# Kernel optimization log

Hardware: AMD Instinct MI355X
Metric: run time of the kernel (lower is better)

## Reference

```python
import jax, jax.numpy as jnp
import numpy as np

N_USERS = 100000
N_ITEMS = 50000
EMB = 64
E_U = 1600000
E_I = 800000
EPS = 1e-12
NEG_SLOPE = 0.01  # torch F.leaky_relu default


def _spmm(rows, cols, vals, x, n):
    # sparse.mm(adj, x): out[r] += vals[e] * x[cols[e]] for each edge e with rows[e]==r
    return jax.ops.segment_sum(vals[:, None] * x[cols], rows, num_segments=n)


def _l2norm(x):
    # F.normalize(x, p=2, dim=1)
    n = jnp.sqrt(jnp.sum(x * x, axis=1, keepdims=True))
    return x / jnp.maximum(n, EPS)


def setup_inputs() -> dict:
    key = jax.random.key(0)
    ks = jax.random.split(key, 16)
    inp = {
        'user_emb': 0.01 * jax.random.normal(ks[0], (N_USERS, EMB), jnp.float32),
        'item_emb': 0.01 * jax.random.normal(ks[1], (N_ITEMS, EMB), jnp.float32),
        'Wu0': jax.random.normal(ks[2], (EMB, EMB), jnp.float32) / np.sqrt(EMB),
        'bu0': jnp.zeros((EMB,), jnp.float32),
        'Wu1': jax.random.normal(ks[3], (EMB, EMB), jnp.float32) / np.sqrt(EMB),
        'bu1': jnp.zeros((EMB,), jnp.float32),
        'Wi0': jax.random.normal(ks[4], (EMB, EMB), jnp.float32) / np.sqrt(EMB),
        'bi0': jnp.zeros((EMB,), jnp.float32),
        'Wi1': jax.random.normal(ks[5], (EMB, EMB), jnp.float32) / np.sqrt(EMB),
        'bi1': jnp.zeros((EMB,), jnp.float32),
        'u_rows': jax.random.randint(ks[6], (E_U,), 0, N_USERS, jnp.int32),
        'u_cols': jax.random.randint(ks[7], (E_U,), 0, N_USERS, jnp.int32),
        'u_vals': jax.random.uniform(ks[8], (E_U,), jnp.float32) / 16.0,
        'i_rows': jax.random.randint(ks[9], (E_I,), 0, N_ITEMS, jnp.int32),
        'i_cols': jax.random.randint(ks[10], (E_I,), 0, N_ITEMS, jnp.int32),
        'i_vals': jax.random.uniform(ks[11], (E_I,), jnp.float32) / 16.0,
    }
    return inp


def reference(user_emb, item_emb, Wu0, bu0, Wu1, bu1, Wi0, bi0, Wi1, bi1,
              u_rows, u_cols, u_vals, i_rows, i_cols, i_vals):
    u = user_emb
    i = item_emb
    u_w = [(Wu0, bu0), (Wu1, bu1)]
    i_w = [(Wi0, bi0), (Wi1, bi1)]
    for l in range(2):
        Wu, bu = u_w[l]
        Wi, bi = i_w[l]
        u = _spmm(u_rows, u_cols, u_vals, u, N_USERS)
        u = jax.nn.leaky_relu(u @ Wu.T + bu, NEG_SLOPE)
        u = _l2norm(u)  # dropout p=0 -> identity
        i = _spmm(i_rows, i_cols, i_vals, i, N_ITEMS)
        i = jax.nn.leaky_relu(i @ Wi.T + bi, NEG_SLOPE)
        i = _l2norm(i)
    return (u, i)
```

## Files before the change

### kernel.cpp

```cpp
#include <hip/hip_runtime.h>
#include <hip/hip_bf16.h>
#include <math.h>

#define EMB 64
#define CAPB 3584
#define CHUNK 4096

typedef __attribute__((ext_vector_type(8))) short bf16x8;
typedef __attribute__((ext_vector_type(4))) float f32x4;

__device__ __forceinline__ ushort bf16_rne(float f) {
    uint u = __float_as_uint(f);
    return (ushort)((u + 0x7fffu + ((u >> 16) & 1u)) >> 16);
}


__device__ __forceinline__ void bin_body(
    const int* __restrict__ rows, const int* __restrict__ cols,
    const float* __restrict__ vals, int nE, int B, int RPB,
    int* gcur, int2* __restrict__ binned, int blk,
    int* cnt, int* sstart, int* lbase, int2* rec, ushort* bkt) {
    int t = threadIdx.x;
    for (int i = t; i < B; i += 256) cnt[i] = 0;
    __syncthreads();
    int c0 = blk * CHUNK;
    int ntot = nE - c0; if (ntot > CHUNK) ntot = CHUNK;
    int bs[16];
#pragma unroll
    for (int j = 0; j < 16; ++j) {
        int idx = c0 + t + j * 256;
        int bsv = -1;
        if (idx < nE) {
            int row = rows[idx];
            int b = row / RPB;
            int inrow = row - b * RPB;
            int slot = atomicAdd(&cnt[b], 1);
            bsv = (b << 21) | (inrow << 13) | slot;
        }
        bs[j] = bsv;
    }
    __syncthreads();
    for (int i = t; i < B; i += 256) {
        int c = cnt[i];
        lbase[i] = c ? atomicAdd(&gcur[i * 16], c) : 0;
    }
    if (t < 64) {
        int carry = 0;
        int nseg = B >> 6;
        for (int seg = 0; seg < nseg; ++seg) {
            int i = seg * 64 + t;
            int v = cnt[i];
            int s = v;
#pragma unroll
            for (int d = 1; d < 64; d <<= 1) {
                int u2 = __shfl_up(s, d);
                if (t >= d) s += u2;
            }
            sstart[i] = carry + s - v;
            carry += __shfl(s, 63);
        }
    }
    __syncthreads();
#pragma unroll
    for (int j = 0; j < 16; ++j) {
        int idx = c0 + t + j * 256;
        if (idx >= nE) continue;
        int bsv = bs[j];
        int b = bsv >> 21, inrow = (bsv >> 13) & 0xFF, slot = bsv & 0x1FFF;
        int col = cols[idx];
        float v = vals[idx];
        int li = sstart[b] + slot;
        rec[li] = make_int2(col | (inrow << 17), __float_as_int(v));
        bkt[li] = (ushort)b;
    }
    __syncthreads();
    for (int i = t; i < ntot; i += 256) {
        int b = bkt[i];
        int pos = lbase[b] + (i - sstart[b]);
        if (pos < CAPB)
            binned[(size_t)b * CAPB + pos] = rec[i];
    }
}

__global__ __launch_bounds__(256) void prep(
    const int* __restrict__ u_rows, const int* __restrict__ u_cols,
    const float* __restrict__ u_vals, int eu, int BU, int RPBU,
    int* gcurU, int2* __restrict__ binnedU, int nbU,
    const int* __restrict__ i_rows, const int* __restrict__ i_cols,
    const float* __restrict__ i_vals, int ei, int BI, int RPBI,
    int* gcurI, int2* __restrict__ binnedI, int nbI,
    const float4* __restrict__ embU, ushort* __restrict__ xbU, long n4u,
    const float4* __restrict__ embI, ushort* __restrict__ xbI, long n4i,
    int nbCast) {
    __shared__ int2 rec[CHUNK];
    __shared__ ushort bkt[CHUNK];
    __shared__ int cnt[512];
    __shared__ int sstart[512];
    __shared__ int lbase[512];
    int b = blockIdx.x;
    if (b < nbU) {
        bin_body(u_rows, u_cols, u_vals, eu, BU, RPBU, gcurU, binnedU, b,
                 cnt, sstart, lbase, rec, bkt);
        return;
    }
    b -= nbU;
    if (b < nbI) {
        bin_body(i_rows, i_cols, i_vals, ei, BI, RPBI, gcurI, binnedI, b,
                 cnt, sstart, lbase, rec, bkt);
        return;
    }
    b -= nbI;
    long tot = n4u + n4i;
    long base = (long)b * 1024 + threadIdx.x;
#pragma unroll
    for (int k = 0; k < 4; ++k) {
        long i = base + k * 256;
        if (i >= tot) return;
        const float4* a; ushort* o; long j;
        if (i < n4u) { a = embU; o = xbU; j = i; }
        else { a = embI; o = xbI; j = i - n4u; }
        float4 v = a[j];
        ushort4 r;
        r.x = bf16_rne(v.x); r.y = bf16_rne(v.y); r.z = bf16_rne(v.z); r.w = bf16_rne(v.w);
        *(ushort4*)(o + j * 4) = r;
    }
}

__device__ __forceinline__ int block_scan_1024(int v, int* wsum) {
    int tid = threadIdx.x, lane = tid & 63, wid = tid >> 6;
    int s = v;
#pragma unroll
    for (int d = 1; d < 64; d <<= 1) {
        int t = __shfl_up(s, d);
        if (lane >= d) s += t;
    }
    if (lane == 63) wsum[wid] = s;
    __syncthreads();
    if (tid < 16) {
        int ws = wsum[tid];
#pragma unroll
        for (int d = 1; d < 16; d <<= 1) {
            int t = __shfl_up(ws, d);
            if (tid >= d) ws += t;
        }
        wsum[tid] = ws;
    }
    __syncthreads();
    int wpref = (wid > 0) ? wsum[wid - 1] : 0;
    return wpref + s;
}

__global__ void scan_buckets(const int* __restrict__ gcurU, int BU, int* cntbU, int* ebaseU,
                             const int* __restrict__ gcurI, int BI, int* cntbI, int* ebaseI) {
    __shared__ int wsum[16];
    const int* gcur; int B; int* cntb; int* ebase;
    if (blockIdx.x == 0) { gcur = gcurU; B = BU; cntb = cntbU; ebase = ebaseU; }
    else { gcur = gcurI; B = BI; cntb = cntbI; ebase = ebaseI; }
    int t = threadIdx.x;
    int v = 0;
    if (t < B) {
        v = gcur[t * 16];
        if (v < 0) v = 0;
        if (v > CAPB) v = CAPB;
    }
    int incl = block_scan_1024(v, wsum);
    if (t < B) { cntb[t] = v; ebase[t] = incl - v; }
}

__global__ __launch_bounds__(256) void finalize_csr(
    const int2* __restrict__ binnedU, const int* __restrict__ cntbU,
    const int* __restrict__ ebaseU, int RPBU, int nu,
    int2* __restrict__ ccvU, int* __restrict__ uoff, int BU,
    const int2* __restrict__ binnedI, const int* __restrict__ cntbI,
    const int* __restrict__ ebaseI, int RPBI, int ni,
    int2* __restrict__ ccvI, int* __restrict__ ioff) {
    __shared__ int2 rec[CAPB];
    __shared__ int cnt_r[256];
    __shared__ int excl[257];
    __shared__ int curs[256];
    int b = blockIdx.x;
    const int2* binned; const int* cntb; const int* ebase; int RPB; int n;
    int2* ccv; int* off;
    if (b < BU) {
        binned = binnedU; cntb = cntbU; ebase = ebaseU; RPB = RPBU; n = nu;
        ccv = ccvU; off = uoff;
    } else {
        b -= BU;
        binned = binnedI; cntb = cntbI; ebase = ebaseI; RPB = RPBI; n = ni;
        ccv = ccvI; off = ioff;
    }
    int t = threadIdx.x;
    int r0 = b * RPB;
    int nrows = n - r0; if (nrows > RPB) nrows = RPB;
    if (nrows <= 0) return;
    int cnt = cntb[b];
    int eb  = ebase[b];
    const int2* src = binned + (size_t)b * CAPB;
    cnt_r[t] = 0;
    __syncthreads();
    for (int p = t; p < cnt; p += 256) {
        int2 r = src[p];
        rec[p] = r;
        atomicAdd(&cnt_r[(r.x >> 17) & 0xFF], 1);
    }
    __syncthreads();
    if (t < 64) {
        int carry = 0;
#pragma unroll
        for (int seg = 0; seg < 4; ++seg) {
            int i = seg * 64 + t;
            int v = cnt_r[i];
            int s = v;
#pragma unroll
            for (int d = 1; d < 64; d <<= 1) {
                int u2 = __shfl_up(s, d);
                if (t >= d) s += u2;
            }
            excl[i] = carry + s - v;
            carry += __shfl(s, 63);
        }
        if (t == 0) excl[256] = carry;
    }
    __syncthreads();
    curs[t] = excl[t];
    if (t < nrows) off[r0 + t] = eb + excl[t];
    if (t == 0 && r0 + nrows == n) off[n] = eb + cnt;
    __syncthreads();
    for (int p = t; p < cnt; p += 256) {
        int2 r = rec[p];
        int inrow = (r.x >> 17) & 0xFF;
        int slot = atomicAdd(&curs[inrow], 1);
        ccv[eb + slot] = make_int2(r.x & 0x1FFFF, r.y);
    }
}


__global__ __launch_bounds__(256, 4) void spmm_mfma(
    const int* __restrict__ uoff, const int2* __restrict__ ccvU,
    const ushort* __restrict__ xu, const float* __restrict__ Wu, const float* __restrict__ bu,
    float* __restrict__ yfu, ushort* __restrict__ ybu, int nu, int ntU,
    const int* __restrict__ ioff, const int2* __restrict__ ccvI,
    const ushort* __restrict__ xi, const float* __restrict__ Wi, const float* __restrict__ bi,
    float* __restrict__ yfi, ushort* __restrict__ ybi, int ni) {
    __shared__ ushort wt[64 * 72];
    __shared__ ushort xt[4 * 16 * 72];
    int tid = threadIdx.x;
    int lane = tid & 63, wid = tid >> 6;
    int q = lane & 15, g = lane >> 4;
    int tile = blockIdx.x;
    const int* off; const int2* ccv; const ushort* x; const float* W; const float* bv;
    float* yf; ushort* yb; int n;
    if (tile < ntU) {
        off = uoff; ccv = ccvU; x = xu; W = Wu; bv = bu; yf = yfu; yb = ybu; n = nu;
    } else {
        tile -= ntU;
        off = ioff; ccv = ccvI; x = xi; W = Wi; bv = bi; yf = yfi; yb = ybi; n = ni;
    }
    for (int idx = tid; idx < EMB * EMB; idx += 256) {
        int r = idx >> 6, c = idx & 63;
        wt[r * 72 + c] = bf16_rne(W[idx]);
    }
    float bias[4];
#pragma unroll
    for (int t = 0; t < 4; ++t) bias[t] = bv[16 * t + q];
    __syncthreads();

    const uint2* xv2 = (const uint2*)x;
    ushort* xw = xt + wid * (16 * 72);
    int rowW = (tile << 6) + wid * 16;

#pragma unroll
    for (int j = 0; j < 4; ++j) {
        int rr = j * 4 + g;
        int row = rowW + rr;
        float av[4] = {0.f, 0.f, 0.f, 0.f};
        if (row < n) {
            int s = off[row], e = off[row + 1];
            for (int p = s; p < e; p += 8) {
                int2 ed[8];
                uint2 gx[8];
#pragma unroll
                for (int k = 0; k < 8; ++k) {
                    int idx = p + k;
                    idx = (idx < e) ? idx : (e - 1);
                    ed[k] = ccv[idx];
                }
#pragma unroll
                for (int k = 0; k < 8; ++k)
                    gx[k] = xv2[(size_t)(uint)ed[k].x * 16 + q];
#pragma unroll
                for (int k = 0; k < 8; ++k) {
                    float v = (p + k < e) ? __int_as_float(ed[k].y) : 0.f;
                    av[0] = fmaf(v, __uint_as_float(gx[k].x << 16), av[0]);
                    av[1] = fmaf(v, __uint_as_float(gx[k].x & 0xffff0000u), av[1]);
                    av[2] = fmaf(v, __uint_as_float(gx[k].y << 16), av[2]);
                    av[3] = fmaf(v, __uint_as_float(gx[k].y & 0xffff0000u), av[3]);
                }
            }
        }
        uint p0 = (uint)bf16_rne(av[0]) | ((uint)bf16_rne(av[1]) << 16);
        uint p1 = (uint)bf16_rne(av[2]) | ((uint)bf16_rne(av[3]) << 16);
        *(uint2*)(xw + rr * 72 + q * 4) = make_uint2(p0, p1);
    }
    __syncthreads();

    f32x4 ac0 = {0.f, 0.f, 0.f, 0.f}, ac1 = ac0, ac2 = ac0, ac3 = ac0;
#pragma unroll
    for (int ks = 0; ks < 2; ++ks) {
        bf16x8 af = *(const bf16x8*)(xw + q * 72 + g * 8 + ks * 32);
        bf16x8 b0 = *(const bf16x8*)(wt + (q +  0) * 72 + g * 8 + ks * 32);
        bf16x8 b1 = *(const bf16x8*)(wt + (q + 16) * 72 + g * 8 + ks * 32);
        bf16x8 b2 = *(const bf16x8*)(wt + (q + 32) * 72 + g * 8 + ks * 32);
        bf16x8 b3 = *(const bf16x8*)(wt + (q + 48) * 72 + g * 8 + ks * 32);
        ac0 = __builtin_amdgcn_mfma_f32_16x16x32_bf16(af, b0, ac0, 0, 0, 0);
        ac1 = __builtin_amdgcn_mfma_f32_16x16x32_bf16(af, b1, ac1, 0, 0, 0);
        ac2 = __builtin_amdgcn_mfma_f32_16x16x32_bf16(af, b2, ac2, 0, 0, 0);
        ac3 = __builtin_amdgcn_mfma_f32_16x16x32_bf16(af, b3, ac3, 0, 0, 0);
    }

    float dv[4][4];
    float ss[4] = {0.f, 0.f, 0.f, 0.f};
#pragma unroll
    for (int t = 0; t < 4; ++t) {
        f32x4 a = (t == 0) ? ac0 : (t == 1) ? ac1 : (t == 2) ? ac2 : ac3;
#pragma unroll
        for (int r = 0; r < 4; ++r) {
            float d = a[r] + bias[t];
            d = (d > 0.f) ? d : 0.01f * d;
            dv[t][r] = d;
            ss[r] = fmaf(d, d, ss[r]);
        }
    }
#pragma unroll
    for (int r = 0; r < 4; ++r) {
        float s2 = ss[r];
        s2 += __shfl_xor(s2, 1);
        s2 += __shfl_xor(s2, 2);
        s2 += __shfl_xor(s2, 4);
        s2 += __shfl_xor(s2, 8);
        float scl = 1.0f / fmaxf(sqrtf(s2), 1e-12f);
        int orow = rowW + g * 4 + r;
        if (orow < n) {
#pragma unroll
            for (int t = 0; t < 4; ++t) {
                float outv = dv[t][r] * scl;
                size_t cidx = (size_t)orow * EMB + 16 * t + q;
                if (yb) yb[cidx] = bf16_rne(outv);
                else    yf[cidx] = outv;
            }
        }
    }
}


extern "C" void kernel_launch(void* const* d_in, const int* in_sizes, int n_in,
                              void* d_out, int out_size, void* d_ws, size_t ws_size,
                              hipStream_t stream) {
    const float* user_emb = (const float*)d_in[0];
    const float* item_emb = (const float*)d_in[1];
    const float* Wu0 = (const float*)d_in[2];
    const float* bu0 = (const float*)d_in[3];
    const float* Wu1 = (const float*)d_in[4];
    const float* bu1 = (const float*)d_in[5];
    const float* Wi0 = (const float*)d_in[6];
    const float* bi0 = (const float*)d_in[7];
    const float* Wi1 = (const float*)d_in[8];
    const float* bi1 = (const float*)d_in[9];
    const int*   u_rows = (const int*)d_in[10];
    const int*   u_cols = (const int*)d_in[11];
    const float* u_vals = (const float*)d_in[12];
    const int*   i_rows = (const int*)d_in[13];
    const int*   i_cols = (const int*)d_in[14];
    const float* i_vals = (const float*)d_in[15];

    const int nu = in_sizes[0] / EMB;
    const int ni = in_sizes[1] / EMB;
    const int eu = in_sizes[10];
    const int ei = in_sizes[13];

    const int BU = 512, BI = 256;
    const int RPBU = (nu + BU - 1) / BU;
    const int RPBI = (ni + BI - 1) / BI;

    float* out_u = (float*)d_out;
    float* out_i = out_u + (size_t)nu * EMB;

    size_t o = 0;
    char* wsb = (char*)d_ws;
    auto carve = [&](size_t bytes) -> void* {
        void* p = wsb + o;
        o += (bytes + 255) & ~(size_t)255;
        return p;
    };
    ushort* xbu0 = (ushort*)carve((size_t)nu * EMB * 2);
    ushort* xbi0 = (ushort*)carve((size_t)ni * EMB * 2);
    size_t binnedU_bytes = (size_t)BU * CAPB * 8;
    size_t binnedI_bytes = (size_t)BI * CAPB * 8;
    size_t xb1_bytes = ((size_t)nu + ni) * EMB * 2;
    size_t shared_bytes = binnedU_bytes + binnedI_bytes;
    if (xb1_bytes > shared_bytes) shared_bytes = xb1_bytes;
    char* regionA = (char*)carve(shared_bytes);
    int2* binnedU = (int2*)regionA;
    int2* binnedI = (int2*)(regionA + binnedU_bytes);
    ushort* xbu1 = (ushort*)regionA;
    ushort* xbi1 = (ushort*)(regionA + (size_t)nu * EMB * 2);
    int2* ccvU  = (int2*)carve((size_t)eu * 8);
    int2* ccvI  = (int2*)carve((size_t)ei * 8);
    int*  uoff  = (int*)carve((size_t)(nu + 1) * 4);
    int*  ioff  = (int*)carve((size_t)(ni + 1) * 4);
    int*  gcur  = (int*)carve((size_t)(BU + BI) * 16 * 4);
    int*  gcurU = gcur;
    int*  gcurI = gcur + (size_t)BU * 16;
    int*  cntbU = (int*)carve((size_t)BU * 4);
    int*  ebaseU= (int*)carve((size_t)BU * 4);
    int*  cntbI = (int*)carve((size_t)BI * 4);
    int*  ebaseI= (int*)carve((size_t)BI * 4);
    (void)ws_size;

    hipMemsetAsync(gcur, 0, (size_t)(BU + BI) * 16 * 4, stream);
    {
        int nbU = (eu + CHUNK - 1) / CHUNK;
        int nbI = (ei + CHUNK - 1) / CHUNK;
        long n4u = (long)nu * EMB / 4, n4i = (long)ni * EMB / 4;
        int nbCast = (int)((n4u + n4i + 1023) / 1024);
        prep<<<nbU + nbI + nbCast, 256, 0, stream>>>(
            u_rows, u_cols, u_vals, eu, BU, RPBU, gcurU, binnedU, nbU,
            i_rows, i_cols, i_vals, ei, BI, RPBI, gcurI, binnedI, nbI,
            (const float4*)user_emb, xbu0, n4u,
            (const float4*)item_emb, xbi0, n4i, nbCast);
    }
    scan_buckets<<<2, 1024, 0, stream>>>(gcurU, BU, cntbU, ebaseU,
                                         gcurI, BI, cntbI, ebaseI);
    finalize_csr<<<BU + BI, 256, 0, stream>>>(
        binnedU, cntbU, ebaseU, RPBU, nu, ccvU, uoff, BU,
        binnedI, cntbI, ebaseI, RPBI, ni, ccvI, ioff);

    int ntU = (nu + 63) >> 6, ntI = (ni + 63) >> 6;
    spmm_mfma<<<ntU + ntI, 256, 0, stream>>>(
        uoff, ccvU, xbu0, Wu0, bu0, nullptr, xbu1, nu, ntU,
        ioff, ccvI, xbi0, Wi0, bi0, nullptr, xbi1, ni);
    spmm_mfma<<<ntU + ntI, 256, 0, stream>>>(
        uoff, ccvU, xbu1, Wu1, bu1, out_u, nullptr, nu, ntU,
        ioff, ccvI, xbi1, Wi1, bi1, out_i, nullptr, ni);
}
```

Baseline: 195.2 us.

## Drop bucket scan kernel and sort CSR in place within padded bins

Removes the scan_buckets launch and the compacted CCV arrays: finalize_csr now reads each bucket's count straight from gcur, sorts edges in place inside the padded binned buffer, and writes per-row (start,end) int2 pairs instead of a global offset array. The SpMM kernels read edges directly from the padded bins using these pairs. This drops one kernel launch and one serialized dependency. The xb1 buffers no longer alias the binned region, which raises workspace use. spmm launch bounds are also raised from 4 to 6 blocks per SM, which may limit registers.

```diff
diff --git a/kernel.cpp b/kernel.cpp
--- a/kernel.cpp
+++ b/kernel.cpp
@@ -126,76 +126,32 @@
     }
 }
 
-__device__ __forceinline__ int block_scan_1024(int v, int* wsum) {
-    int tid = threadIdx.x, lane = tid & 63, wid = tid >> 6;
-    int s = v;
-#pragma unroll
-    for (int d = 1; d < 64; d <<= 1) {
-        int t = __shfl_up(s, d);
-        if (lane >= d) s += t;
-    }
-    if (lane == 63) wsum[wid] = s;
-    __syncthreads();
-    if (tid < 16) {
-        int ws = wsum[tid];
-#pragma unroll
-        for (int d = 1; d < 16; d <<= 1) {
-            int t = __shfl_up(ws, d);
-            if (tid >= d) ws += t;
-        }
-        wsum[tid] = ws;
-    }
-    __syncthreads();
-    int wpref = (wid > 0) ? wsum[wid - 1] : 0;
-    return wpref + s;
-}
-
-__global__ void scan_buckets(const int* __restrict__ gcurU, int BU, int* cntbU, int* ebaseU,
-                             const int* __restrict__ gcurI, int BI, int* cntbI, int* ebaseI) {
-    __shared__ int wsum[16];
-    const int* gcur; int B; int* cntb; int* ebase;
-    if (blockIdx.x == 0) { gcur = gcurU; B = BU; cntb = cntbU; ebase = ebaseU; }
-    else { gcur = gcurI; B = BI; cntb = cntbI; ebase = ebaseI; }
-    int t = threadIdx.x;
-    int v = 0;
-    if (t < B) {
-        v = gcur[t * 16];
-        if (v < 0) v = 0;
-        if (v > CAPB) v = CAPB;
-    }
-    int incl = block_scan_1024(v, wsum);
-    if (t < B) { cntb[t] = v; ebase[t] = incl - v; }
-}
 
 __global__ __launch_bounds__(256) void finalize_csr(
-    const int2* __restrict__ binnedU, const int* __restrict__ cntbU,
-    const int* __restrict__ ebaseU, int RPBU, int nu,
-    int2* __restrict__ ccvU, int* __restrict__ uoff, int BU,
-    const int2* __restrict__ binnedI, const int* __restrict__ cntbI,
-    const int* __restrict__ ebaseI, int RPBI, int ni,
-    int2* __restrict__ ccvI, int* __restrict__ ioff) {
+    int2* __restrict__ binnedU, const int* __restrict__ gcurU, int RPBU, int nu,
+    int2* __restrict__ offseU, int BU,
+    int2* __restrict__ binnedI, const int* __restrict__ gcurI, int RPBI, int ni,
+    int2* __restrict__ offseI) {
     __shared__ int2 rec[CAPB];
     __shared__ int cnt_r[256];
     __shared__ int excl[257];
     __shared__ int curs[256];
     int b = blockIdx.x;
-    const int2* binned; const int* cntb; const int* ebase; int RPB; int n;
-    int2* ccv; int* off;
+    int2* binned; const int* gcur; int RPB; int n; int2* offse;
     if (b < BU) {
-        binned = binnedU; cntb = cntbU; ebase = ebaseU; RPB = RPBU; n = nu;
-        ccv = ccvU; off = uoff;
+        binned = binnedU; gcur = gcurU; RPB = RPBU; n = nu; offse = offseU;
     } else {
         b -= BU;
-        binned = binnedI; cntb = cntbI; ebase = ebaseI; RPB = RPBI; n = ni;
-        ccv = ccvI; off = ioff;
+        binned = binnedI; gcur = gcurI; RPB = RPBI; n = ni; offse = offseI;
     }
     int t = threadIdx.x;
     int r0 = b * RPB;
     int nrows = n - r0; if (nrows > RPB) nrows = RPB;
     if (nrows <= 0) return;
-    int cnt = cntb[b];
-    int eb  = ebase[b];
-    const int2* src = binned + (size_t)b * CAPB;
+    int cnt = gcur[b * 16];
+    if (cnt > CAPB) cnt = CAPB;
+    int2* src = binned + (size_t)b * CAPB;
+    int B0 = b * CAPB;
     cnt_r[t] = 0;
     __syncthreads();
     for (int p = t; p < cnt; p += 256) {
@@ -223,23 +179,22 @@
     }
     __syncthreads();
     curs[t] = excl[t];
-    if (t < nrows) off[r0 + t] = eb + excl[t];
-    if (t == 0 && r0 + nrows == n) off[n] = eb + cnt;
+    if (t < nrows) offse[r0 + t] = make_int2(B0 + excl[t], B0 + excl[t + 1]);
     __syncthreads();
     for (int p = t; p < cnt; p += 256) {
         int2 r = rec[p];
         int inrow = (r.x >> 17) & 0xFF;
         int slot = atomicAdd(&curs[inrow], 1);
-        ccv[eb + slot] = make_int2(r.x & 0x1FFFF, r.y);
-    }
-}
-
-
-__global__ __launch_bounds__(256, 4) void spmm_mfma(
-    const int* __restrict__ uoff, const int2* __restrict__ ccvU,
+        src[slot] = make_int2(r.x & 0x1FFFF, r.y);
+    }
+}
+
+
+__global__ __launch_bounds__(256, 6) void spmm_mfma(
+    const int2* __restrict__ offseU, const int2* __restrict__ ccvU,
     const ushort* __restrict__ xu, const float* __restrict__ Wu, const float* __restrict__ bu,
     float* __restrict__ yfu, ushort* __restrict__ ybu, int nu, int ntU,
-    const int* __restrict__ ioff, const int2* __restrict__ ccvI,
+    const int2* __restrict__ offseI, const int2* __restrict__ ccvI,
     const ushort* __restrict__ xi, const float* __restrict__ Wi, const float* __restrict__ bi,
     float* __restrict__ yfi, ushort* __restrict__ ybi, int ni) {
     __shared__ ushort wt[64 * 72];
@@ -248,13 +203,13 @@
     int lane = tid & 63, wid = tid >> 6;
     int q = lane & 15, g = lane >> 4;
     int tile = blockIdx.x;
-    const int* off; const int2* ccv; const ushort* x; const float* W; const float* bv;
+    const int2* offse; const int2* ccv; const ushort* x; const float* W; const float* bv;
     float* yf; ushort* yb; int n;
     if (tile < ntU) {
-        off = uoff; ccv = ccvU; x = xu; W = Wu; bv = bu; yf = yfu; yb = ybu; n = nu;
+        offse = offseU; ccv = ccvU; x = xu; W = Wu; bv = bu; yf = yfu; yb = ybu; n = nu;
     } else {
         tile -= ntU;
-        off = ioff; ccv = ccvI; x = xi; W = Wi; bv = bi; yf = yfi; yb = ybi; n = ni;
+        offse = offseI; ccv = ccvI; x = xi; W = Wi; bv = bi; yf = yfi; yb = ybi; n = ni;
     }
     for (int idx = tid; idx < EMB * EMB; idx += 256) {
         int r = idx >> 6, c = idx & 63;
@@ -275,7 +230,8 @@
         int row = rowW + rr;
         float av[4] = {0.f, 0.f, 0.f, 0.f};
         if (row < n) {
-            int s = off[row], e = off[row + 1];
+            int2 se = offse[row];
+            int s = se.x, e = se.y;
             for (int p = s; p < e; p += 8) {
                 int2 ed[8];
                 uint2 gx[8];
@@ -394,27 +350,15 @@
     };
     ushort* xbu0 = (ushort*)carve((size_t)nu * EMB * 2);
     ushort* xbi0 = (ushort*)carve((size_t)ni * EMB * 2);
-    size_t binnedU_bytes = (size_t)BU * CAPB * 8;
-    size_t binnedI_bytes = (size_t)BI * CAPB * 8;
-    size_t xb1_bytes = ((size_t)nu + ni) * EMB * 2;
-    size_t shared_bytes = binnedU_bytes + binnedI_bytes;
-    if (xb1_bytes > shared_bytes) shared_bytes = xb1_bytes;
-    char* regionA = (char*)carve(shared_bytes);
-    int2* binnedU = (int2*)regionA;
-    int2* binnedI = (int2*)(regionA + binnedU_bytes);
-    ushort* xbu1 = (ushort*)regionA;
-    ushort* xbi1 = (ushort*)(regionA + (size_t)nu * EMB * 2);
-    int2* ccvU  = (int2*)carve((size_t)eu * 8);
-    int2* ccvI  = (int2*)carve((size_t)ei * 8);
-    int*  uoff  = (int*)carve((size_t)(nu + 1) * 4);
-    int*  ioff  = (int*)carve((size_t)(ni + 1) * 4);
+    int2* binnedU = (int2*)carve((size_t)BU * CAPB * 8);
+    int2* binnedI = (int2*)carve((size_t)BI * CAPB * 8);
+    ushort* xbu1 = (ushort*)carve((size_t)nu * EMB * 2);
+    ushort* xbi1 = (ushort*)carve((size_t)ni * EMB * 2);
+    int2* offseU = (int2*)carve((size_t)nu * 8);
+    int2* offseI = (int2*)carve((size_t)ni * 8);
     int*  gcur  = (int*)carve((size_t)(BU + BI) * 16 * 4);
     int*  gcurU = gcur;
     int*  gcurI = gcur + (size_t)BU * 16;
-    int*  cntbU = (int*)carve((size_t)BU * 4);
-    int*  ebaseU= (int*)carve((size_t)BU * 4);
-    int*  cntbI = (int*)carve((size_t)BI * 4);
-    int*  ebaseI= (int*)carve((size_t)BI * 4);
     (void)ws_size;
 
     hipMemsetAsync(gcur, 0, (size_t)(BU + BI) * 16 * 4, stream);
@@ -429,17 +373,15 @@
             (const float4*)user_emb, xbu0, n4u,
             (const float4*)item_emb, xbi0, n4i, nbCast);
     }
-    scan_buckets<<<2, 1024, 0, stream>>>(gcurU, BU, cntbU, ebaseU,
-                                         gcurI, BI, cntbI, ebaseI);
     finalize_csr<<<BU + BI, 256, 0, stream>>>(
-        binnedU, cntbU, ebaseU, RPBU, nu, ccvU, uoff, BU,
-        binnedI, cntbI, ebaseI, RPBI, ni, ccvI, ioff);
+        binnedU, gcurU, RPBU, nu, offseU, BU,
+        binnedI, gcurI, RPBI, ni, offseI);
 
     int ntU = (nu + 63) >> 6, ntI = (ni + 63) >> 6;
     spmm_mfma<<<ntU + ntI, 256, 0, stream>>>(
-        uoff, ccvU, xbu0, Wu0, bu0, nullptr, xbu1, nu, ntU,
-        ioff, ccvI, xbi0, Wi0, bi0, nullptr, xbi1, ni);
+        offseU, binnedU, xbu0, Wu0, bu0, nullptr, xbu1, nu, ntU,
+        offseI, binnedI, xbi0, Wi0, bi0, nullptr, xbi1, ni);
     spmm_mfma<<<ntU + ntI, 256, 0, stream>>>(
-        uoff, ccvU, xbu1, Wu1, bu1, out_u, nullptr, nu, ntU,
-        ioff, ccvI, xbi1, Wi1, bi1, out_i, nullptr, ni);
-}
+        offseU, binnedU, xbu1, Wu1, bu1, out_u, nullptr, nu, ntU,
+        offseI, binnedI, xbi1, Wi1, bi1, out_i, nullptr, ni);
+}
```

Result: faster. 190.7 us (-2.3%).
